# Optimization experiments

Measured on AMD Instinct MI355X. Metric: run time of the kernel, lower is better.

Reference implementation:

```python
import jax, jax.numpy as jnp
import numpy as np

NH = 12  # num_heads

def setup_inputs() -> dict:
    key = jax.random.key(0)
    ks = jax.random.split(key, 8)
    B, N, C = 8, 1024, 768
    d = C // NH  # head_dim == qk_head_dim (qk_head_dim=None)
    s = 0.02
    return {
        "x": jax.random.normal(ks[0], (B, N, C), jnp.float32),
        "Wq": jax.random.normal(ks[1], (C, NH * d), jnp.float32) * s,
        "Wk": jax.random.normal(ks[2], (C, NH * d), jnp.float32) * s,
        "Wv": jax.random.normal(ks[3], (C, C), jnp.float32) * s,
        "Wproj": jax.random.normal(ks[4], (C, C), jnp.float32) * s,
        "proj_b": jax.random.normal(ks[5], (C,), jnp.float32) * s,
        "attn_bias": jax.random.normal(ks[6], (N, N), jnp.float32) * s,
        "head_bias": jax.random.normal(ks[7], (NH, N, N), jnp.float32) * s,
    }

def reference(x, Wq, Wk, Wv, Wproj, proj_b, attn_bias, head_bias):
    B, N, C = x.shape
    d = C // NH
    scale = d ** -0.5
    # projections: [B,N,C] -> [B,nh,N,d]
    q = jnp.einsum('bnc,ce->bne', x, Wq).reshape(B, N, NH, d).transpose(0, 2, 1, 3)
    k = jnp.einsum('bnc,ce->bne', x, Wk).reshape(B, N, NH, d).transpose(0, 2, 1, 3)
    v = jnp.einsum('bnc,ce->bne', x, Wv).reshape(B, N, NH, d).transpose(0, 2, 1, 3)
    # scaled scores + global bias + per-head bias
    scores = jnp.einsum('bhnd,bhmd->bhnm', q * scale, k)
    scores = scores + attn_bias[None, None] + head_bias[None]
    attn = jax.nn.softmax(scores, axis=-1)  # [B,nh,N,N]
    out = jnp.einsum('bhnm,bhmd->bhnd', attn, v)
    out = out.transpose(0, 2, 1, 3).reshape(B, N, C)
    out = jnp.einsum('bnc,ce->bne', out, Wproj) + proj_b
    return out, attn
```

## Files before the change

### kernel.cpp

```cpp
#include <hip/hip_runtime.h>
#include <hip/hip_bf16.h>
#include <cstddef>

#define B_   8
#define N_   1024
#define C_   768
#define NH_  12
#define HD_  64
#define M_   (B_ * N_)

typedef __attribute__((ext_vector_type(8))) short  short8;
typedef __attribute__((ext_vector_type(4))) float  f32x4;

__device__ __forceinline__ unsigned short f2b(float f) {
    union { float f; unsigned u; } v; v.f = f;
    unsigned u = v.u;
    return (unsigned short)((u + 0x7FFFu + ((u >> 16) & 1u)) >> 16);
}
__device__ __forceinline__ float b2f(unsigned short s) {
    union { unsigned u; float f; } v; v.u = ((unsigned)s) << 16;
    return v.f;
}
__device__ __forceinline__ ushort2 pk2(float a, float b) {
    __hip_bfloat162 t = __float22bfloat162_rn(make_float2(a, b));
    return *(ushort2*)&t;
}
__device__ __forceinline__ void barrier_lds() {
    asm volatile("s_waitcnt lgkmcnt(0)" ::: "memory");
    __builtin_amdgcn_sched_barrier(0);
    __builtin_amdgcn_s_barrier();
    __builtin_amdgcn_sched_barrier(0);
}

__global__ __launch_bounds__(256) void cast_x_kernel(const float* __restrict__ x,
                                                     unsigned short* __restrict__ xb) {
    const int n4 = M_ * C_ / 4;
    for (int i = blockIdx.x * blockDim.x + threadIdx.x; i < n4; i += gridDim.x * blockDim.x) {
        float4 v = ((const float4*)x)[i];
        ushort2 lo = pk2(v.x, v.y), hi = pk2(v.z, v.w);
        ushort4 o; o.x = lo.x; o.y = lo.y; o.z = hi.x; o.w = hi.y;
        ((ushort4*)xb)[i] = o;
    }
}

__global__ __launch_bounds__(256) void bias_combine_kernel(
    const float* __restrict__ ab, const float* __restrict__ hbias,
    unsigned short* __restrict__ bc) {
    const int total4 = NH_ * N_ * N_ / 4;
    const int qm4 = N_ * N_ / 4;
    for (int i = blockIdx.x * blockDim.x + threadIdx.x; i < total4; i += gridDim.x * blockDim.x) {
        int rem = i % qm4;
        float4 a = ((const float4*)ab)[rem];
        float4 h = ((const float4*)hbias)[i];
        ushort2 lo = pk2(a.x + h.x, a.y + h.y), hi = pk2(a.z + h.z, a.w + h.w);
        ushort4 o; o.x = lo.x; o.y = lo.y; o.z = hi.x; o.w = hi.y;
        ((ushort4*)bc)[i] = o;
    }
}

__global__ __launch_bounds__(256) void transpose_cast_kernel(
    const float* __restrict__ w0, const float* __restrict__ w1,
    const float* __restrict__ w2, const float* __restrict__ w3,
    unsigned short* __restrict__ t0, unsigned short* __restrict__ t1,
    unsigned short* __restrict__ t2, unsigned short* __restrict__ t3) {
    const int z = blockIdx.z;
    const float* src = (z == 0) ? w0 : (z == 1) ? w1 : (z == 2) ? w2 : w3;
    unsigned short* dst = (z == 0) ? t0 : (z == 1) ? t1 : (z == 2) ? t2 : t3;
    __shared__ float tile[32][33];
    const int r0 = blockIdx.y * 32, c0 = blockIdx.x * 32;
    const int tx = threadIdx.x & 31, ty = threadIdx.x >> 5;
    #pragma unroll
    for (int p = 0; p < 4; ++p)
        tile[ty + 8 * p][tx] = src[(size_t)(r0 + ty + 8 * p) * C_ + c0 + tx];
    __syncthreads();
    #pragma unroll
    for (int p = 0; p < 4; ++p)
        dst[(size_t)(c0 + ty + 8 * p) * C_ + r0 + tx] = f2b(tile[tx][ty + 8 * p]);
}

__global__ __launch_bounds__(256) void qkv_gemm(
    const unsigned short* __restrict__ A,
    const unsigned short* __restrict__ W0, const unsigned short* __restrict__ W1,
    const unsigned short* __restrict__ W2,
    unsigned short* __restrict__ o0, unsigned short* __restrict__ o1,
    unsigned short* __restrict__ o2) {
    __shared__ unsigned short As[128][40];
    __shared__ unsigned short Bs[64][40];
    const int z = blockIdx.z;
    const unsigned short* Bt = (z == 0) ? W0 : (z == 1) ? W1 : W2;
    const int tid = threadIdx.x;
    const int wid = tid >> 6, lane = tid & 63;
    const int ln = lane & 15, g = lane >> 4;
    const int wm = wid >> 1, wn = wid & 1;
    const int bm = blockIdx.y * 128, bn = blockIdx.x * 64;

    f32x4 acc[4][2];
    #pragma unroll
    for (int i = 0; i < 4; ++i)
        #pragma unroll
        for (int j = 0; j < 2; ++j) acc[i][j] = (f32x4)0.f;

    for (int k0 = 0; k0 < C_; k0 += 32) {
        #pragma unroll
        for (int p = 0; p < 2; ++p) {
            int idx = tid + p * 256;
            int row = idx >> 2, ch = idx & 3;
            *(int4*)&As[row][ch * 8] =
                *(const int4*)&A[(size_t)(bm + row) * C_ + k0 + ch * 8];
        }
        {
            int n = tid >> 2, ch = tid & 3;
            *(int4*)&Bs[n][ch * 8] =
                *(const int4*)&Bt[(size_t)(bn + n) * C_ + k0 + ch * 8];
        }
        __syncthreads();
        short8 a[4], b[2];
        #pragma unroll
        for (int mt = 0; mt < 4; ++mt)
            a[mt] = *(const short8*)&As[wm * 64 + mt * 16 + ln][g * 8];
        #pragma unroll
        for (int nt = 0; nt < 2; ++nt)
            b[nt] = *(const short8*)&Bs[wn * 32 + nt * 16 + ln][g * 8];
        #pragma unroll
        for (int mt = 0; mt < 4; ++mt)
            #pragma unroll
            for (int nt = 0; nt < 2; ++nt)
                acc[mt][nt] = __builtin_amdgcn_mfma_f32_16x16x32_bf16(
                    a[mt], b[nt], acc[mt][nt], 0, 0, 0);
        __syncthreads();
    }

    unsigned short* outp = (z == 0) ? o0 : (z == 1) ? o1 : o2;
    #pragma unroll
    for (int mt = 0; mt < 4; ++mt) {
        #pragma unroll
        for (int nt = 0; nt < 2; ++nt) {
            f32x4 c = acc[mt][nt];
            int rowb = bm + wm * 64 + mt * 16 + g * 4;
            int col  = bn + wn * 32 + nt * 16 + ln;
            int hh = col >> 6, dd = col & 63;
            if (z < 2) {
                #pragma unroll
                for (int i = 0; i < 4; ++i) {
                    int row = rowb + i;
                    int bb = row >> 10, n = row & 1023;
                    outp[((size_t)(bb * NH_ + hh) * N_ + n) * HD_ + dd] = f2b(c[i]);
                }
            } else {
                int bb = rowb >> 10, n0 = rowb & 1023;
                ushort2 lo = pk2(c[0], c[1]), hi = pk2(c[2], c[3]);
                ushort4 pk; pk.x = lo.x; pk.y = lo.y; pk.z = hi.x; pk.w = hi.y;
                *(ushort4*)&outp[((size_t)(bb * NH_ + hh) * HD_ + dd) * N_ + n0] = pk;
            }
        }
    }
}

__global__ __launch_bounds__(256) void proj_gemm(
    const unsigned short* __restrict__ A, const unsigned short* __restrict__ Bt,
    const float* __restrict__ bias, float* __restrict__ outp) {
    __shared__ unsigned short As[128][40];
    __shared__ unsigned short Bs[64][40];
    const int tid = threadIdx.x;
    const int wid = tid >> 6, lane = tid & 63;
    const int ln = lane & 15, g = lane >> 4;
    const int wm = wid >> 1, wn = wid & 1;
    const int bm = blockIdx.y * 128, bn = blockIdx.x * 64;

    f32x4 acc[4][2];
    #pragma unroll
    for (int i = 0; i < 4; ++i)
        #pragma unroll
        for (int j = 0; j < 2; ++j) acc[i][j] = (f32x4)0.f;

    for (int k0 = 0; k0 < C_; k0 += 32) {
        #pragma unroll
        for (int p = 0; p < 2; ++p) {
            int idx = tid + p * 256;
            int row = idx >> 2, ch = idx & 3;
            *(int4*)&As[row][ch * 8] =
                *(const int4*)&A[(size_t)(bm + row) * C_ + k0 + ch * 8];
        }
        {
            int n = tid >> 2, ch = tid & 3;
            *(int4*)&Bs[n][ch * 8] =
                *(const int4*)&Bt[(size_t)(bn + n) * C_ + k0 + ch * 8];
        }
        __syncthreads();
        short8 a[4], b[2];
        #pragma unroll
        for (int mt = 0; mt < 4; ++mt)
            a[mt] = *(const short8*)&As[wm * 64 + mt * 16 + ln][g * 8];
        #pragma unroll
        for (int nt = 0; nt < 2; ++nt)
            b[nt] = *(const short8*)&Bs[wn * 32 + nt * 16 + ln][g * 8];
        #pragma unroll
        for (int mt = 0; mt < 4; ++mt)
            #pragma unroll
            for (int nt = 0; nt < 2; ++nt)
                acc[mt][nt] = __builtin_amdgcn_mfma_f32_16x16x32_bf16(
                    a[mt], b[nt], acc[mt][nt], 0, 0, 0);
        __syncthreads();
    }

    #pragma unroll
    for (int mt = 0; mt < 4; ++mt) {
        #pragma unroll
        for (int nt = 0; nt < 2; ++nt) {
            f32x4 c = acc[mt][nt];
            int rowb = bm + wm * 64 + mt * 16 + g * 4;
            int col  = bn + wn * 32 + nt * 16 + ln;
            float bb = bias[col];
            #pragma unroll
            for (int i = 0; i < 4; ++i)
                outp[(size_t)(rowb + i) * C_ + col] = c[i] + bb;
        }
    }
}

__global__ __launch_bounds__(512) void attn_fused(
    const unsigned short* __restrict__ qh, const unsigned short* __restrict__ kh,
    const unsigned short* __restrict__ vt,
    const unsigned short* __restrict__ bias_c,
    float* __restrict__ attn_out, unsigned short* __restrict__ hb) {
    __shared__ unsigned short sc[32 * 1024];
    __shared__ float sinv[32];
    const int id = blockIdx.x;
    const int xcd = id & 7;
    const int b = (id >> 3) & 7;
    const int qbh = ((id >> 6) << 3) + xcd;
    const int qb0 = (qbh / NH_) * 32;
    const int h = qbh % NH_;
    const int bh = b * NH_ + h;
    const int tid = threadIdx.x;
    const int wid = tid >> 6, lane = tid & 63;
    const int ln = lane & 15, g = lane >> 4;

    #define SCP(row, m) ((unsigned short*)((char*)sc + (row) * 2048 + \
                         (((m) * 2) ^ (((row) & 7) << 4))))

    {
        short8 qf[2][2];
        #pragma unroll
        for (int Mt = 0; Mt < 2; ++Mt)
            #pragma unroll
            for (int kc = 0; kc < 2; ++kc)
                qf[Mt][kc] = *(const short8*)&qh[
                    ((size_t)bh * N_ + qb0 + Mt * 16 + ln) * HD_ + kc * 32 + g * 8];
        const int mb = wid * 128;
        const unsigned short* kbase = kh + (size_t)bh * N_ * HD_;
        short8 k0 = *(const short8*)&kbase[(size_t)(mb + ln) * HD_ + g * 8];
        short8 k1 = *(const short8*)&kbase[(size_t)(mb + ln) * HD_ + 32 + g * 8];
        for (int mt = 0; mt < 8; ++mt) {
            const int m0 = mb + mt * 16;
            const int m1 = (mt < 7) ? m0 + 16 : m0;
            short8 n0 = *(const short8*)&kbase[(size_t)(m1 + ln) * HD_ + g * 8];
            short8 n1 = *(const short8*)&kbase[(size_t)(m1 + ln) * HD_ + 32 + g * 8];
            #pragma unroll
            for (int Mt = 0; Mt < 2; ++Mt) {
                f32x4 s = (f32x4)0.f;
                s = __builtin_amdgcn_mfma_f32_16x16x32_bf16(k0, qf[Mt][0], s, 0, 0, 0);
                s = __builtin_amdgcn_mfma_f32_16x16x32_bf16(k1, qf[Mt][1], s, 0, 0, 0);
                const int mrow = m0 + g * 4;
                ushort2 lo = pk2(s[0] * 0.125f, s[1] * 0.125f);
                ushort2 hi = pk2(s[2] * 0.125f, s[3] * 0.125f);
                ushort4 pk; pk.x = lo.x; pk.y = lo.y; pk.z = hi.x; pk.w = hi.y;
                *(ushort4*)SCP(Mt * 16 + ln, mrow) = pk;
            }
            k0 = n0; k1 = n1;
        }
    }
    barrier_lds();

    {
        const int r = tid >> 4, t16 = tid & 15;
        const unsigned short* brow = bias_c + ((size_t)h * N_ + qb0 + r) * N_;
        f32x4 sv[16];
        float mx = -1e30f;
        #pragma unroll
        for (int j = 0; j < 16; ++j) {
            ushort4 er = *(const ushort4*)SCP(r, t16 * 4 + j * 64);
            ushort4 bb = *(const ushort4*)&brow[t16 * 4 + j * 64];
            sv[j][0] = b2f(er.x) + b2f(bb.x);
            sv[j][1] = b2f(er.y) + b2f(bb.y);
            sv[j][2] = b2f(er.z) + b2f(bb.z);
            sv[j][3] = b2f(er.w) + b2f(bb.w);
            mx = fmaxf(fmaxf(fmaxf(mx, sv[j][0]), fmaxf(sv[j][1], sv[j][2])), sv[j][3]);
        }
        #pragma unroll
        for (int off = 8; off; off >>= 1) mx = fmaxf(mx, __shfl_xor(mx, off, 16));
        float sum = 0.f;
        #pragma unroll
        for (int j = 0; j < 16; ++j) {
            float e0 = __expf(sv[j][0] - mx);
            float e1 = __expf(sv[j][1] - mx);
            float e2 = __expf(sv[j][2] - mx);
            float e3 = __expf(sv[j][3] - mx);
            sv[j][0] = e0; sv[j][1] = e1; sv[j][2] = e2; sv[j][3] = e3;
            sum += (e0 + e1) + (e2 + e3);
            ushort2 lo = pk2(e0, e1), hi = pk2(e2, e3);
            ushort4 pk; pk.x = lo.x; pk.y = lo.y; pk.z = hi.x; pk.w = hi.y;
            *(ushort4*)SCP(r, t16 * 4 + j * 64) = pk;
        }
        #pragma unroll
        for (int off = 8; off; off >>= 1) sum += __shfl_xor(sum, off, 16);
        const float inv = 1.f / sum;
        if (t16 == 0) sinv[r] = inv;
        float* arow = attn_out + ((size_t)bh * N_ + qb0 + r) * N_;
        #pragma unroll
        for (int j = 0; j < 16; ++j) {
            f32x4 o;
            o[0] = sv[j][0] * inv; o[1] = sv[j][1] * inv;
            o[2] = sv[j][2] * inv; o[3] = sv[j][3] * inv;
            __builtin_nontemporal_store(o, (f32x4*)&arow[t16 * 4 + j * 64]);
        }
    }
    barrier_lds();

    {
        const int Mt = wid >> 2, nt = wid & 3;
        const unsigned short* vrow = vt + ((size_t)bh * HD_ + nt * 16 + ln) * N_;
        f32x4 acc = (f32x4)0.f;
        short8 pa = *(const short8*)SCP(Mt * 16 + ln, g * 8);
        short8 vb = *(const short8*)&vrow[g * 8];
        for (int kt = 0; kt < 32; ++kt) {
            const int knext = (kt < 31) ? kt + 1 : kt;
            short8 npa = *(const short8*)SCP(Mt * 16 + ln, knext * 32 + g * 8);
            short8 nvb = *(const short8*)&vrow[knext * 32 + g * 8];
            acc = __builtin_amdgcn_mfma_f32_16x16x32_bf16(pa, vb, acc, 0, 0, 0);
            pa = npa; vb = nvb;
        }
        #pragma unroll
        for (int i = 0; i < 4; ++i) {
            int q = qb0 + Mt * 16 + g * 4 + i;
            float o = acc[i] * sinv[Mt * 16 + g * 4 + i];
            hb[(size_t)((b << 10) + q) * C_ + h * HD_ + nt * 16 + ln] = f2b(o);
        }
    }
    #undef SCP
}

extern "C" void kernel_launch(void* const* d_in, const int* in_sizes, int n_in,
                              void* d_out, int out_size, void* d_ws, size_t ws_size,
                              hipStream_t stream) {
    const float* x         = (const float*)d_in[0];
    const float* Wq        = (const float*)d_in[1];
    const float* Wk        = (const float*)d_in[2];
    const float* Wv        = (const float*)d_in[3];
    const float* Wproj     = (const float*)d_in[4];
    const float* proj_b    = (const float*)d_in[5];
    const float* attn_bias = (const float*)d_in[6];
    const float* head_bias = (const float*)d_in[7];

    float* out  = (float*)d_out;
    float* attn = out + (size_t)B_ * N_ * C_;

    unsigned short* ws = (unsigned short*)d_ws;
    const size_t SZ_X = (size_t)M_ * C_;
    const size_t SZ_W = (size_t)C_ * C_;
    unsigned short* xb  = ws;
    unsigned short* wqt = xb + SZ_X;
    unsigned short* wkt = wqt + SZ_W;
    unsigned short* wvt = wkt + SZ_W;
    unsigned short* wpt = wvt + SZ_W;
    unsigned short* qh  = wpt + SZ_W;
    unsigned short* khd = qh + SZ_X;
    unsigned short* vtp = khd + SZ_X;
    unsigned short* bc  = vtp + SZ_X;
    unsigned short* hb  = xb;

    cast_x_kernel<<<2048, 256, 0, stream>>>(x, xb);
    bias_combine_kernel<<<2048, 256, 0, stream>>>(attn_bias, head_bias, bc);
    transpose_cast_kernel<<<dim3(24, 24, 4), 256, 0, stream>>>(
        Wq, Wk, Wv, Wproj, wqt, wkt, wvt, wpt);

    qkv_gemm<<<dim3(C_ / 64, M_ / 128, 3), 256, 0, stream>>>(
        xb, wqt, wkt, wvt, qh, khd, vtp);

    attn_fused<<<dim3(B_ * (N_ / 32) * NH_), 512, 0, stream>>>(
        qh, khd, vtp, bc, attn, hb);

    proj_gemm<<<dim3(C_ / 64, M_ / 128), 256, 0, stream>>>(hb, wpt, proj_b, out);
}
```

Measured before the change: 309.7 us.

## Widen softmax vector accesses and split PV over K with LDS reduction

The softmax pass now handles 8 elements per access (16-byte LDS and bias loads and stores) instead of 4, halving the number of memory instructions. The P·V stage is reorganized so each wave computes both 16-row query tiles against one V fragment, reusing each V load twice, and splits the K dimension across two wave groups whose partial sums are combined through a small LDS buffer behind an extra barrier. The cost is more LDS and an added synchronization in exchange for fewer global V loads and shorter MFMA chains per wave.

```diff
diff --git a/kernel.cpp b/kernel.cpp
--- a/kernel.cpp
+++ b/kernel.cpp
@@ -224,6 +224,7 @@
     const unsigned short* __restrict__ bias_c,
     float* __restrict__ attn_out, unsigned short* __restrict__ hb) {
     __shared__ unsigned short sc[32 * 1024];
+    __shared__ f32x4 red[4][64][2];
     __shared__ float sinv[32];
     const int id = blockIdx.x;
     const int xcd = id & 7;
@@ -275,66 +276,87 @@
     {
         const int r = tid >> 4, t16 = tid & 15;
         const unsigned short* brow = bias_c + ((size_t)h * N_ + qb0 + r) * N_;
-        f32x4 sv[16];
+        float sv[8][8];
         float mx = -1e30f;
         #pragma unroll
-        for (int j = 0; j < 16; ++j) {
-            ushort4 er = *(const ushort4*)SCP(r, t16 * 4 + j * 64);
-            ushort4 bb = *(const ushort4*)&brow[t16 * 4 + j * 64];
-            sv[j][0] = b2f(er.x) + b2f(bb.x);
-            sv[j][1] = b2f(er.y) + b2f(bb.y);
-            sv[j][2] = b2f(er.z) + b2f(bb.z);
-            sv[j][3] = b2f(er.w) + b2f(bb.w);
-            mx = fmaxf(fmaxf(fmaxf(mx, sv[j][0]), fmaxf(sv[j][1], sv[j][2])), sv[j][3]);
+        for (int j = 0; j < 8; ++j) {
+            short8 er = *(const short8*)SCP(r, t16 * 8 + j * 128);
+            short8 bb = *(const short8*)&brow[t16 * 8 + j * 128];
+            #pragma unroll
+            for (int e = 0; e < 8; ++e) {
+                float s = b2f((unsigned short)er[e]) + b2f((unsigned short)bb[e]);
+                sv[j][e] = s;
+                mx = fmaxf(mx, s);
+            }
         }
         #pragma unroll
         for (int off = 8; off; off >>= 1) mx = fmaxf(mx, __shfl_xor(mx, off, 16));
         float sum = 0.f;
         #pragma unroll
-        for (int j = 0; j < 16; ++j) {
-            float e0 = __expf(sv[j][0] - mx);
-            float e1 = __expf(sv[j][1] - mx);
-            float e2 = __expf(sv[j][2] - mx);
-            float e3 = __expf(sv[j][3] - mx);
-            sv[j][0] = e0; sv[j][1] = e1; sv[j][2] = e2; sv[j][3] = e3;
-            sum += (e0 + e1) + (e2 + e3);
-            ushort2 lo = pk2(e0, e1), hi = pk2(e2, e3);
-            ushort4 pk; pk.x = lo.x; pk.y = lo.y; pk.z = hi.x; pk.w = hi.y;
-            *(ushort4*)SCP(r, t16 * 4 + j * 64) = pk;
+        for (int j = 0; j < 8; ++j) {
+            #pragma unroll
+            for (int e = 0; e < 8; ++e) {
+                float ev = __expf(sv[j][e] - mx);
+                sv[j][e] = ev;
+                sum += ev;
+            }
+            ushort2 p0 = pk2(sv[j][0], sv[j][1]);
+            ushort2 p1 = pk2(sv[j][2], sv[j][3]);
+            ushort2 p2 = pk2(sv[j][4], sv[j][5]);
+            ushort2 p3 = pk2(sv[j][6], sv[j][7]);
+            short8 pk;
+            pk[0] = p0.x; pk[1] = p0.y; pk[2] = p1.x; pk[3] = p1.y;
+            pk[4] = p2.x; pk[5] = p2.y; pk[6] = p3.x; pk[7] = p3.y;
+            *(short8*)SCP(r, t16 * 8 + j * 128) = pk;
         }
         #pragma unroll
         for (int off = 8; off; off >>= 1) sum += __shfl_xor(sum, off, 16);
         const float inv = 1.f / sum;
         if (t16 == 0) sinv[r] = inv;
-        float* arow = attn_out + ((size_t)bh * N_ + qb0 + r) * N_;
-        #pragma unroll
-        for (int j = 0; j < 16; ++j) {
-            f32x4 o;
-            o[0] = sv[j][0] * inv; o[1] = sv[j][1] * inv;
-            o[2] = sv[j][2] * inv; o[3] = sv[j][3] * inv;
-            __builtin_nontemporal_store(o, (f32x4*)&arow[t16 * 4 + j * 64]);
+        float* arow = attn_out + ((size_t)bh * N_ + qb0 + r) * N_ + t16 * 8;
+        #pragma unroll
+        for (int j = 0; j < 8; ++j) {
+            f32x4 o0, o1;
+            o0[0] = sv[j][0] * inv; o0[1] = sv[j][1] * inv;
+            o0[2] = sv[j][2] * inv; o0[3] = sv[j][3] * inv;
+            o1[0] = sv[j][4] * inv; o1[1] = sv[j][5] * inv;
+            o1[2] = sv[j][6] * inv; o1[3] = sv[j][7] * inv;
+            __builtin_nontemporal_store(o0, (f32x4*)&arow[j * 128]);
+            __builtin_nontemporal_store(o1, (f32x4*)&arow[j * 128 + 4]);
         }
     }
     barrier_lds();
 
     {
-        const int Mt = wid >> 2, nt = wid & 3;
+        const int nt = wid & 3, khf = wid >> 2;
         const unsigned short* vrow = vt + ((size_t)bh * HD_ + nt * 16 + ln) * N_;
-        f32x4 acc = (f32x4)0.f;
-        short8 pa = *(const short8*)SCP(Mt * 16 + ln, g * 8);
-        short8 vb = *(const short8*)&vrow[g * 8];
-        for (int kt = 0; kt < 32; ++kt) {
-            const int knext = (kt < 31) ? kt + 1 : kt;
-            short8 npa = *(const short8*)SCP(Mt * 16 + ln, knext * 32 + g * 8);
-            short8 nvb = *(const short8*)&vrow[knext * 32 + g * 8];
-            acc = __builtin_amdgcn_mfma_f32_16x16x32_bf16(pa, vb, acc, 0, 0, 0);
-            pa = npa; vb = nvb;
-        }
-        #pragma unroll
-        for (int i = 0; i < 4; ++i) {
-            int q = qb0 + Mt * 16 + g * 4 + i;
-            float o = acc[i] * sinv[Mt * 16 + g * 4 + i];
-            hb[(size_t)((b << 10) + q) * C_ + h * HD_ + nt * 16 + ln] = f2b(o);
+        f32x4 acc0 = (f32x4)0.f, acc1 = (f32x4)0.f;
+        #pragma unroll
+        for (int kt = 0; kt < 16; ++kt) {
+            const int ktg = khf * 16 + kt;
+            short8 vb = *(const short8*)&vrow[ktg * 32 + g * 8];
+            short8 pa0 = *(const short8*)SCP(ln, ktg * 32 + g * 8);
+            short8 pa1 = *(const short8*)SCP(16 + ln, ktg * 32 + g * 8);
+            acc0 = __builtin_amdgcn_mfma_f32_16x16x32_bf16(pa0, vb, acc0, 0, 0, 0);
+            acc1 = __builtin_amdgcn_mfma_f32_16x16x32_bf16(pa1, vb, acc1, 0, 0, 0);
+        }
+        if (khf == 1) {
+            red[nt][lane][0] = acc0;
+            red[nt][lane][1] = acc1;
+        }
+        barrier_lds();
+        if (khf == 0) {
+            f32x4 r0 = red[nt][lane][0], r1 = red[nt][lane][1];
+            acc0 += r0; acc1 += r1;
+            const int col = h * HD_ + nt * 16 + ln;
+            #pragma unroll
+            for (int i = 0; i < 4; ++i) {
+                int q0 = qb0 + g * 4 + i;
+                hb[(size_t)((b << 10) + q0) * C_ + col] =
+                    f2b(acc0[i] * sinv[g * 4 + i]);
+                hb[(size_t)((b << 10) + q0 + 16) * C_ + col] =
+                    f2b(acc1[i] * sinv[16 + g * 4 + i]);
+            }
         }
     }
     #undef SCP
```

Measured after the change: 312.9 us. About the same (+1.0%).

## Double attention block to 1024 threads and overlap attn store with PV matmul

Applied to the files above, without the earlier changes.

Raises the attention block to 1024 threads, giving each wave a single query tile in the QK^T stage. Softmax now keeps no per-thread register array: it stages biased scores and exponentials as bf16 in LDS. After softmax, waves 0-7 run the PV MFMA while waves 8-15 read the bf16 exponentials back from LDS and write the normalized fp32 attention matrix, so the large global store runs alongside the matmul. In exchange, the returned attention probabilities are rounded to bf16 before normalization, there are extra LDS round trips, and the launch_bounds(1024, 8) hint adds register pressure.

```diff
diff --git a/kernel.cpp b/kernel.cpp
--- a/kernel.cpp
+++ b/kernel.cpp
@@ -24,6 +24,14 @@
 __device__ __forceinline__ ushort2 pk2(float a, float b) {
     __hip_bfloat162 t = __float22bfloat162_rn(make_float2(a, b));
     return *(ushort2*)&t;
+}
+__device__ __forceinline__ short8 pk8(const float* s) {
+    ushort2 p0 = pk2(s[0], s[1]), p1 = pk2(s[2], s[3]);
+    ushort2 p2 = pk2(s[4], s[5]), p3 = pk2(s[6], s[7]);
+    short8 w;
+    w[0] = p0.x; w[1] = p0.y; w[2] = p1.x; w[3] = p1.y;
+    w[4] = p2.x; w[5] = p2.y; w[6] = p3.x; w[7] = p3.y;
+    return w;
 }
 __device__ __forceinline__ void barrier_lds() {
     asm volatile("s_waitcnt lgkmcnt(0)" ::: "memory");
@@ -218,7 +226,7 @@
     }
 }
 
-__global__ __launch_bounds__(512) void attn_fused(
+__global__ __launch_bounds__(1024, 8) void attn_fused(
     const unsigned short* __restrict__ qh, const unsigned short* __restrict__ kh,
     const unsigned short* __restrict__ vt,
     const unsigned short* __restrict__ bias_c,
@@ -240,85 +248,74 @@
                          (((m) * 2) ^ (((row) & 7) << 4))))
 
     {
-        short8 qf[2][2];
-        #pragma unroll
-        for (int Mt = 0; Mt < 2; ++Mt)
-            #pragma unroll
-            for (int kc = 0; kc < 2; ++kc)
-                qf[Mt][kc] = *(const short8*)&qh[
-                    ((size_t)bh * N_ + qb0 + Mt * 16 + ln) * HD_ + kc * 32 + g * 8];
-        const int mb = wid * 128;
+        const int Mt = wid & 1;
+        const int mb = (wid >> 1) * 128;
+        short8 qf0 = *(const short8*)&qh[
+            ((size_t)bh * N_ + qb0 + Mt * 16 + ln) * HD_ + g * 8];
+        short8 qf1 = *(const short8*)&qh[
+            ((size_t)bh * N_ + qb0 + Mt * 16 + ln) * HD_ + 32 + g * 8];
         const unsigned short* kbase = kh + (size_t)bh * N_ * HD_;
         short8 k0 = *(const short8*)&kbase[(size_t)(mb + ln) * HD_ + g * 8];
         short8 k1 = *(const short8*)&kbase[(size_t)(mb + ln) * HD_ + 32 + g * 8];
+        #pragma unroll
         for (int mt = 0; mt < 8; ++mt) {
             const int m0 = mb + mt * 16;
             const int m1 = (mt < 7) ? m0 + 16 : m0;
             short8 n0 = *(const short8*)&kbase[(size_t)(m1 + ln) * HD_ + g * 8];
             short8 n1 = *(const short8*)&kbase[(size_t)(m1 + ln) * HD_ + 32 + g * 8];
+            f32x4 s = (f32x4)0.f;
+            s = __builtin_amdgcn_mfma_f32_16x16x32_bf16(k0, qf0, s, 0, 0, 0);
+            s = __builtin_amdgcn_mfma_f32_16x16x32_bf16(k1, qf1, s, 0, 0, 0);
+            const int mrow = m0 + g * 4;
+            ushort2 lo = pk2(s[0] * 0.125f, s[1] * 0.125f);
+            ushort2 hi = pk2(s[2] * 0.125f, s[3] * 0.125f);
+            ushort4 pk; pk.x = lo.x; pk.y = lo.y; pk.z = hi.x; pk.w = hi.y;
+            *(ushort4*)SCP(Mt * 16 + ln, mrow) = pk;
+            k0 = n0; k1 = n1;
+        }
+    }
+    barrier_lds();
+
+    {
+        const int r = tid >> 5, t32 = tid & 31;
+        const unsigned short* brow = bias_c + ((size_t)h * N_ + qb0 + r) * N_;
+        float mx = -1e30f;
+        #pragma unroll
+        for (int j = 0; j < 4; ++j) {
+            const int m = t32 * 8 + j * 256;
+            short8 er = *(const short8*)SCP(r, m);
+            short8 bb = *(const short8*)&brow[m];
+            float s[8];
             #pragma unroll
-            for (int Mt = 0; Mt < 2; ++Mt) {
-                f32x4 s = (f32x4)0.f;
-                s = __builtin_amdgcn_mfma_f32_16x16x32_bf16(k0, qf[Mt][0], s, 0, 0, 0);
-                s = __builtin_amdgcn_mfma_f32_16x16x32_bf16(k1, qf[Mt][1], s, 0, 0, 0);
-                const int mrow = m0 + g * 4;
-                ushort2 lo = pk2(s[0] * 0.125f, s[1] * 0.125f);
-                ushort2 hi = pk2(s[2] * 0.125f, s[3] * 0.125f);
-                ushort4 pk; pk.x = lo.x; pk.y = lo.y; pk.z = hi.x; pk.w = hi.y;
-                *(ushort4*)SCP(Mt * 16 + ln, mrow) = pk;
+            for (int e = 0; e < 8; ++e) {
+                s[e] = b2f((unsigned short)er[e]) + b2f((unsigned short)bb[e]);
+                mx = fmaxf(mx, s[e]);
             }
-            k0 = n0; k1 = n1;
-        }
+            *(short8*)SCP(r, m) = pk8(s);
+        }
+        #pragma unroll
+        for (int off = 16; off; off >>= 1) mx = fmaxf(mx, __shfl_xor(mx, off, 32));
+        float sum = 0.f;
+        #pragma unroll
+        for (int j = 0; j < 4; ++j) {
+            const int m = t32 * 8 + j * 256;
+            short8 sr = *(const short8*)SCP(r, m);
+            float e[8];
+            #pragma unroll
+            for (int k = 0; k < 8; ++k) {
+                e[k] = __expf(b2f((unsigned short)sr[k]) - mx);
+                sum += e[k];
+            }
+            *(short8*)SCP(r, m) = pk8(e);
+        }
+        #pragma unroll
+        for (int off = 16; off; off >>= 1) sum += __shfl_xor(sum, off, 32);
+        if (t32 == 0) sinv[r] = 1.f / sum;
     }
     barrier_lds();
 
-    {
-        const int r = tid >> 4, t16 = tid & 15;
-        const unsigned short* brow = bias_c + ((size_t)h * N_ + qb0 + r) * N_;
-        f32x4 sv[16];
-        float mx = -1e30f;
-        #pragma unroll
-        for (int j = 0; j < 16; ++j) {
-            ushort4 er = *(const ushort4*)SCP(r, t16 * 4 + j * 64);
-            ushort4 bb = *(const ushort4*)&brow[t16 * 4 + j * 64];
-            sv[j][0] = b2f(er.x) + b2f(bb.x);
-            sv[j][1] = b2f(er.y) + b2f(bb.y);
-            sv[j][2] = b2f(er.z) + b2f(bb.z);
-            sv[j][3] = b2f(er.w) + b2f(bb.w);
-            mx = fmaxf(fmaxf(fmaxf(mx, sv[j][0]), fmaxf(sv[j][1], sv[j][2])), sv[j][3]);
-        }
-        #pragma unroll
-        for (int off = 8; off; off >>= 1) mx = fmaxf(mx, __shfl_xor(mx, off, 16));
-        float sum = 0.f;
-        #pragma unroll
-        for (int j = 0; j < 16; ++j) {
-            float e0 = __expf(sv[j][0] - mx);
-            float e1 = __expf(sv[j][1] - mx);
-            float e2 = __expf(sv[j][2] - mx);
-            float e3 = __expf(sv[j][3] - mx);
-            sv[j][0] = e0; sv[j][1] = e1; sv[j][2] = e2; sv[j][3] = e3;
-            sum += (e0 + e1) + (e2 + e3);
-            ushort2 lo = pk2(e0, e1), hi = pk2(e2, e3);
-            ushort4 pk; pk.x = lo.x; pk.y = lo.y; pk.z = hi.x; pk.w = hi.y;
-            *(ushort4*)SCP(r, t16 * 4 + j * 64) = pk;
-        }
-        #pragma unroll
-        for (int off = 8; off; off >>= 1) sum += __shfl_xor(sum, off, 16);
-        const float inv = 1.f / sum;
-        if (t16 == 0) sinv[r] = inv;
-        float* arow = attn_out + ((size_t)bh * N_ + qb0 + r) * N_;
-        #pragma unroll
-        for (int j = 0; j < 16; ++j) {
-            f32x4 o;
-            o[0] = sv[j][0] * inv; o[1] = sv[j][1] * inv;
-            o[2] = sv[j][2] * inv; o[3] = sv[j][3] * inv;
-            __builtin_nontemporal_store(o, (f32x4*)&arow[t16 * 4 + j * 64]);
-        }
-    }
-    barrier_lds();
-
-    {
-        const int Mt = wid >> 2, nt = wid & 3;
+    if (wid < 8) {
+        const int nt = wid & 3, Mt = wid >> 2;
         const unsigned short* vrow = vt + ((size_t)bh * HD_ + nt * 16 + ln) * N_;
         f32x4 acc = (f32x4)0.f;
         short8 pa = *(const short8*)SCP(Mt * 16 + ln, g * 8);
@@ -335,6 +332,28 @@
             int q = qb0 + Mt * 16 + g * 4 + i;
             float o = acc[i] * sinv[Mt * 16 + g * 4 + i];
             hb[(size_t)((b << 10) + q) * C_ + h * HD_ + nt * 16 + ln] = f2b(o);
+        }
+    } else {
+        const int t = tid - 512;
+        const int r2 = t >> 4;
+        const int t16 = t & 15;
+        const float inv = sinv[r2];
+        float* arow = attn_out + ((size_t)bh * N_ + qb0 + r2) * N_;
+        #pragma unroll
+        for (int jj = 0; jj < 8; ++jj) {
+            const int m = t16 * 8 + jj * 128;
+            short8 ev = *(const short8*)SCP(r2, m);
+            f32x4 o0, o1;
+            o0[0] = b2f((unsigned short)ev[0]) * inv;
+            o0[1] = b2f((unsigned short)ev[1]) * inv;
+            o0[2] = b2f((unsigned short)ev[2]) * inv;
+            o0[3] = b2f((unsigned short)ev[3]) * inv;
+            o1[0] = b2f((unsigned short)ev[4]) * inv;
+            o1[1] = b2f((unsigned short)ev[5]) * inv;
+            o1[2] = b2f((unsigned short)ev[6]) * inv;
+            o1[3] = b2f((unsigned short)ev[7]) * inv;
+            __builtin_nontemporal_store(o0, (f32x4*)&arow[m]);
+            __builtin_nontemporal_store(o1, (f32x4*)&arow[m + 4]);
         }
     }
     #undef SCP
@@ -377,7 +396,7 @@
     qkv_gemm<<<dim3(C_ / 64, M_ / 128, 3), 256, 0, stream>>>(
         xb, wqt, wkt, wvt, qh, khd, vtp);
 
-    attn_fused<<<dim3(B_ * (N_ / 32) * NH_), 512, 0, stream>>>(
+    attn_fused<<<dim3(B_ * (N_ / 32) * NH_), 1024, 0, stream>>>(
         qh, khd, vtp, bc, attn, hb);
 
     proj_gemm<<<dim3(C_ / 64, M_ / 128), 256, 0, stream>>>(hb, wpt, proj_b, out);
```

After: 370.3 us. 19.5% more time.
